# Performance work log

Measured on AMD Instinct MI355X. Metric: run time of the kernel, lower is better.

Reference implementation:

```python
import jax, jax.numpy as jnp
import numpy as np

B, C, L, D = 8, 32, 2048, 128
R, H = 8, 4  # num_routers, num_heads


def setup_inputs() -> dict:
    key = jax.random.key(0)
    ks = jax.random.split(key, 20)
    p = lambda k, shape: jax.random.normal(k, shape, dtype=jnp.float32) * 0.02
    inp = {
        "Z": jax.random.normal(ks[0], (B, C, L, D), dtype=jnp.float32),
        "router": p(ks[1], (R, D)),
        # router_sender projections (d_model -> d_model, torch Linear stored as x@W+b)
        "Wq1": p(ks[2], (D, D)), "bq1": jnp.zeros((D,), jnp.float32),
        "Wk1": p(ks[3], (D, D)), "bk1": jnp.zeros((D,), jnp.float32),
        "Wv1": p(ks[4], (D, D)), "bv1": jnp.zeros((D,), jnp.float32),
        "Wo1": p(ks[5], (D, D)), "bo1": jnp.zeros((D,), jnp.float32),
        # router_receiver projections
        "Wq2": p(ks[6], (D, D)), "bq2": jnp.zeros((D,), jnp.float32),
        "Wk2": p(ks[7], (D, D)), "bk2": jnp.zeros((D,), jnp.float32),
        "Wv2": p(ks[8], (D, D)), "bv2": jnp.zeros((D,), jnp.float32),
        "Wo2": p(ks[9], (D, D)), "bo2": jnp.zeros((D,), jnp.float32),
        # LayerNorm
        "gamma": jnp.ones((D,), jnp.float32),
        "beta": jnp.zeros((D,), jnp.float32),
    }
    return inp


def _cross_attn(q_in, k_in, v_in, Wq, bq, Wk, bk, Wv, bv, Wo, bo):
    # Informer FullAttention + AttentionLayer (dropout=0)
    Bn, Lq, Dm = q_in.shape
    Lk = k_in.shape[1]
    dh = Dm // H
    q = (q_in @ Wq + bq).reshape(Bn, Lq, H, dh)
    k = (k_in @ Wk + bk).reshape(Bn, Lk, H, dh)
    v = (v_in @ Wv + bv).reshape(Bn, Lk, H, dh)
    scale = 1.0 / np.sqrt(dh)
    scores = jnp.einsum("blhe,bshe->bhls", q, k) * scale
    A = jax.nn.softmax(scores, axis=-1)
    out = jnp.einsum("bhls,bshd->blhd", A, v).reshape(Bn, Lq, Dm)
    return out @ Wo + bo


def _layernorm(x, gamma, beta, eps=1e-5):
    mu = jnp.mean(x, axis=-1, keepdims=True)
    var = jnp.mean(jnp.square(x - mu), axis=-1, keepdims=True)
    return (x - mu) * jax.lax.rsqrt(var + eps) * gamma + beta


def reference(Z, router, Wq1, bq1, Wk1, bk1, Wv1, bv1, Wo1, bo1,
              Wq2, bq2, Wk2, bk2, Wv2, bv2, Wo2, bo2, gamma, beta):
    Bz, Cz, Lz, Dz = Z.shape
    x = Z.reshape(Bz * Cz, Lz, Dz)
    batch_router = jnp.broadcast_to(router[None], (Bz * Cz, R, Dz))
    # stage 1: routers attend to the sequence (R x L)
    router_buffer = _cross_attn(batch_router, x, x,
                                Wq1, bq1, Wk1, bk1, Wv1, bv1, Wo1, bo1)
    # stage 2: sequence attends to routers (L x R)
    router_receive = _cross_attn(x, router_buffer, router_buffer,
                                 Wq2, bq2, Wk2, bk2, Wv2, bv2, Wo2, bo2)
    out = _layernorm(x + router_receive, gamma, beta)
    return out.reshape(Bz, Cz, Lz, Dz)
```

## Files before the change

kernel.cpp:

```cpp
#include <hip/hip_runtime.h>

typedef float f4_t __attribute__((ext_vector_type(4)));
typedef __bf16 bf8_t __attribute__((ext_vector_type(8)));
typedef __bf16 bf4_t __attribute__((ext_vector_type(4)));

#define MFMA16(a,b,c) __builtin_amdgcn_mfma_f32_16x16x32_bf16((a),(b),(c),0,0,0)

static constexpr float kScale = 0.17677669529663687f;

__device__ __forceinline__ void bar_lds() {
  asm volatile("s_waitcnt lgkmcnt(0)" ::: "memory");
  __builtin_amdgcn_s_barrier();
}

__global__ __launch_bounds__(256) void k0_fold(
    const float* __restrict__ router, const float* __restrict__ Wq1,
    const float* __restrict__ bq1, const float* __restrict__ Wk1,
    const float* __restrict__ bk1, __bf16* __restrict__ q1t,
    float* __restrict__ c1)
{
  __shared__ float q1[8][132];
  const int t = threadIdx.x, b = blockIdx.x;
  {
    const int dp = t & 127, rh = t >> 7;
    float acc[4] = {0.f, 0.f, 0.f, 0.f};
#pragma unroll 4
    for (int e = 0; e < 128; ++e) {
      float wq = Wq1[e*128 + dp];
#pragma unroll
      for (int i = 0; i < 4; ++i)
        acc[i] += router[(rh*4 + i)*128 + e] * wq;
    }
#pragma unroll
    for (int i = 0; i < 4; ++i)
      q1[rh*4 + i][dp] = acc[i] + bq1[dp];
  }
  __syncthreads();
  {
    const int j = t & 31, h = j >> 3, r = j & 7;
    const int e = b*8 + (t >> 5);
    f4_t qv[8];
#pragma unroll
    for (int d4 = 0; d4 < 8; ++d4)
      qv[d4] = *(const f4_t*)&q1[r][h*32 + d4*4];
    float acc = 0.f;
#pragma unroll
    for (int d4 = 0; d4 < 8; ++d4) {
      f4_t wv = *(const f4_t*)(Wk1 + e*128 + h*32 + d4*4);
#pragma unroll
      for (int i = 0; i < 4; ++i) acc += qv[d4][i] * wv[i];
    }
    q1t[j*128 + e] = (__bf16)(acc * kScale);
  }
  if (b == 0 && t < 32) {
    int h = t >> 3, r = t & 7;
    float acc = 0.f;
    for (int d = 0; d < 32; ++d) acc += q1[r][h*32 + d] * bk1[h*32 + d];
    c1[t] = acc * kScale;
  }
}

__global__ __launch_bounds__(512) void k1_stage1(
    const float* __restrict__ Z, const __bf16* __restrict__ q1t_g,
    const float* __restrict__ c1_g, float* __restrict__ xap,
    float* __restrict__ lp, __bf16* __restrict__ xws)
{
  __shared__ __bf16 xb[64][136];
  __shared__ __bf16 xT[128][72];
  __shared__ __bf16 PT[32][72];
  __shared__ float lds_l[32];

  const int tid = threadIdx.x;
  const int bid = blockIdx.x;
  const float* xbase = Z + (size_t)bid * (256 * 128);
  __bf16* xwb = xws + (size_t)bid * (256 * 128);

  if (tid < 32) lds_l[tid] = 0.f;

  const int lane = tid & 63;
  const int w = tid >> 6;
  const int lc = lane & 15;
  const int lg = lane >> 4;
  const int ms = w >> 2;
  const int ns = w & 3;
  float c1v[4];
#pragma unroll
  for (int r2 = 0; r2 < 4; ++r2) c1v[r2] = c1_g[ms*16 + lg*4 + r2];
  bf8_t aq[4];
#pragma unroll
  for (int ks = 0; ks < 4; ++ks)
    aq[ks] = *(const bf8_t*)(q1t_g + (ms*16 + lc)*128 + ks*32 + lg*8);

  const f4_t fzero = {0.f, 0.f, 0.f, 0.f};
  f4_t accxa[2] = { fzero, fzero };
  float Lacc[4] = {0.f, 0.f, 0.f, 0.f};

  const int srow = tid >> 4;
  const int sd0  = (tid & 15) << 3;

  f4_t zr[4];
#pragma unroll
  for (int i = 0; i < 2; ++i) {
    const float* p = xbase + (srow + 32*i)*128 + sd0;
    zr[i*2]   = __builtin_nontemporal_load((const f4_t*)p);
    zr[i*2+1] = __builtin_nontemporal_load((const f4_t*)(p + 4));
  }

  bar_lds();

  for (int tile = 0; tile < 4; ++tile) {
#pragma unroll
    for (int i = 0; i < 2; ++i) {
      int pos = srow + 32*i;
      f4_t v0 = zr[i*2], v1 = zr[i*2+1];
      bf8_t b8 = { (__bf16)v0.x, (__bf16)v0.y, (__bf16)v0.z, (__bf16)v0.w,
                   (__bf16)v1.x, (__bf16)v1.y, (__bf16)v1.z, (__bf16)v1.w };
      *(bf8_t*)&xb[pos][sd0] = b8;
      *(bf8_t*)(xwb + (tile*64 + pos)*128 + sd0) = b8;
    }
    bar_lds();

    if (tile < 3) {
      const float* xt = xbase + (tile + 1) * (64 * 128);
#pragma unroll
      for (int i = 0; i < 2; ++i) {
        const float* p = xt + (srow + 32*i)*128 + sd0;
        zr[i*2]   = __builtin_nontemporal_load((const f4_t*)p);
        zr[i*2+1] = __builtin_nontemporal_load((const f4_t*)(p + 4));
      }
    }

#pragma unroll
    for (int s = 0; s < 2; ++s) {
      int u = tid + s*512;
      int dim = u & 127, pb = (u >> 7) << 3;
      bf8_t t8;
#pragma unroll
      for (int p = 0; p < 8; ++p) t8[p] = xb[pb + p][dim];
      *(bf8_t*)&xT[dim][pb] = t8;
    }
    f4_t sacc = fzero;
#pragma unroll
    for (int ks = 0; ks < 4; ++ks) {
      bf8_t b = *(const bf8_t*)&xb[ns*16 + lc][ks*32 + lg*8];
      sacc = MFMA16(aq[ks], b, sacc);
    }
    const int posn = ns*16 + lc;
#pragma unroll
    for (int r2 = 0; r2 < 4; ++r2) {
      float p = __expf(sacc[r2] + c1v[r2]);
      Lacc[r2] += p;
      PT[ms*16 + lg*4 + r2][posn] = (__bf16)p;
    }
    bar_lds();

#pragma unroll
    for (int nt = 0; nt < 2; ++nt) {
      const int dimt = (ns << 1) + nt;
#pragma unroll
      for (int ks = 0; ks < 2; ++ks) {
        bf8_t a = *(const bf8_t*)&xT[dimt*16 + lc][ks*32 + lg*8];
        bf8_t b = *(const bf8_t*)&PT[ms*16 + lc][ks*32 + lg*8];
        accxa[nt] = MFMA16(a, b, accxa[nt]);
      }
    }
  }

#pragma unroll
  for (int r2 = 0; r2 < 4; ++r2) {
    float v = Lacc[r2];
    v += __shfl_xor(v, 1);
    v += __shfl_xor(v, 2);
    v += __shfl_xor(v, 4);
    v += __shfl_xor(v, 8);
    if (lc == 0) atomicAdd(&lds_l[ms*16 + lg*4 + r2], v);
  }
  bar_lds();

  float* xo = xap + (size_t)bid * 4096;
  const int jrow = ms*16 + lc;
#pragma unroll
  for (int nt = 0; nt < 2; ++nt) {
    const int dim0 = ((ns << 1) + nt)*16 + lg*4;
    *(f4_t*)(xo + jrow*128 + dim0) = accxa[nt];
  }
  if (tid < 32) lp[bid*32 + tid] = lds_l[tid];
}

__global__ __launch_bounds__(512) void k2_stage2(
    const __bf16* __restrict__ xws, const float* __restrict__ xap,
    const float* __restrict__ lp,
    const float* __restrict__ Wv1, const float* __restrict__ bv1,
    const float* __restrict__ Wo1, const float* __restrict__ bo1,
    const float* __restrict__ Wk2, const float* __restrict__ bk2,
    const float* __restrict__ Wv2, const float* __restrict__ bv2,
    const float* __restrict__ Wq2, const float* __restrict__ bq2,
    const float* __restrict__ Wo2, const float* __restrict__ bo2,
    const float* __restrict__ gamma, const float* __restrict__ beta,
    float* __restrict__ out)
{
  __shared__ __align__(16) char smem[64896];
  __bf16 (*xb)[136]  = (__bf16 (*)[136])(smem);
  __bf16 (*P2)[40]   = (__bf16 (*)[40])(smem + 34816);
  __bf16 (*ktL)[136] = (__bf16 (*)[136])(smem + 45056);
  __bf16 (*vtL)[40]  = (__bf16 (*)[40])(smem + 53760);
  float* c2L  = (float*)(smem + 64000);
  float* invl = (float*)(smem + 64128);
  float (*xaT)[33]   = (float (*)[33])(smem);
  float (*out1T)[13] = (float (*)[13])(smem + 16896);
  float (*rbT)[13]   = (float (*)[13])(smem + 23552);
  float (*k2s)[140]  = (float (*)[140])(smem);
  float (*v2s)[140]  = (float (*)[140])(smem + 4480);

  const int tid = threadIdx.x;
  const int blk = blockIdx.x;
  const int batch = blk >> 1;

  const int lane = tid & 63;
  const int w = tid >> 6;
  const int lc = lane & 15;
  const int lg = lane >> 4;

  int spos[4], sd[4];
#pragma unroll
  for (int j = 0; j < 4; ++j) {
    int c = lane + j*64;
    spos[j] = w*16 + (c >> 4);
    sd[j]   = (c & 15) << 3;
  }
  const size_t base0 = (size_t)blk * 8 * 16384;
  uint4 zx[4];
#pragma unroll
  for (int j = 0; j < 4; ++j)
    zx[j] = *(const uint4*)(xws + base0 + spos[j]*128 + sd[j]);

#pragma unroll
  for (int i = 0; i < 8; ++i) {
    int idx = tid + i*512;
    int j = idx >> 7, e = idx & 127;
    float s = 0.f;
#pragma unroll
    for (int k = 0; k < 8; ++k)
      s += xap[(size_t)(batch*8 + k) * 4096 + idx];
    xaT[e][j] = s;
  }
  if (tid < 32) {
    float s = 0.f;
#pragma unroll
    for (int k = 0; k < 8; ++k) s += lp[(batch*8 + k)*32 + tid];
    invl[tid] = 1.f / s;
  }
  bar_lds();
  {
    const int hd = tid & 127, rh = tid >> 7, h = hd >> 5;
    const int j0 = h*8 + rh*2;
    float acc[2] = {0.f, 0.f};
#pragma unroll 4
    for (int e = 0; e < 128; ++e) {
      float wv = Wv1[e*128 + hd];
      acc[0] += xaT[e][j0] * wv;
      acc[1] += xaT[e][j0 + 1] * wv;
    }
    float bv = bv1[hd];
    out1T[hd][rh*2]     = acc[0] * invl[j0] + bv;
    out1T[hd][rh*2 + 1] = acc[1] * invl[j0 + 1] + bv;
  }
  bar_lds();
  {
    const int e2 = tid & 127, rh = tid >> 7;
    float acc[2] = {0.f, 0.f};
#pragma unroll 4
    for (int hd = 0; hd < 128; ++hd) {
      float wo = Wo1[hd*128 + e2];
      acc[0] += out1T[hd][rh*2] * wo;
      acc[1] += out1T[hd][rh*2 + 1] * wo;
    }
    float bo = bo1[e2];
    rbT[e2][rh*2]     = acc[0] + bo;
    rbT[e2][rh*2 + 1] = acc[1] + bo;
  }
  bar_lds();
  {
    const int hd = tid & 127, q = tid >> 7;
    const int sel = q >> 1, r0 = (q & 1) * 4;
    const float* W  = sel ? Wv2 : Wk2;
    const float* bb = sel ? bv2 : bk2;
    float (*dst)[140] = sel ? v2s : k2s;
    float bbv = bb[hd];
    float acc[4] = {bbv, bbv, bbv, bbv};
#pragma unroll 4
    for (int e = 0; e < 128; ++e) {
      float wv = W[e*128 + hd];
#pragma unroll
      for (int i = 0; i < 4; ++i) acc[i] += rbT[e][r0 + i] * wv;
    }
#pragma unroll
    for (int i = 0; i < 4; ++i) dst[r0 + i][hd] = acc[i];
  }
  bar_lds();
  {
    const int j = tid & 31, h = j >> 3, r = j & 7;
    const int esub = tid >> 5;
    f4_t k2v[8], v2v[8];
#pragma unroll
    for (int d4 = 0; d4 < 8; ++d4) {
      k2v[d4] = *(const f4_t*)&k2s[r][h*32 + d4*4];
      v2v[d4] = *(const f4_t*)&v2s[r][h*32 + d4*4];
    }
#pragma unroll
    for (int ei = 0; ei < 8; ++ei) {
      const int e = esub + ei*16;
      float acck = 0.f, accv = 0.f;
#pragma unroll
      for (int d4 = 0; d4 < 8; ++d4) {
        f4_t wq = *(const f4_t*)(Wq2 + e*128 + h*32 + d4*4);
#pragma unroll
        for (int i = 0; i < 4; ++i) {
          acck += wq[i] * k2v[d4][i];
          accv += v2v[d4][i] * Wo2[(h*32 + d4*4 + i)*128 + e];
        }
      }
      ktL[j][e] = (__bf16)(acck * kScale);
      vtL[e][j] = (__bf16)accv;
    }
    if (tid < 32) {
      int hh = tid >> 3, rr = tid & 7;
      float acc = 0.f;
#pragma unroll
      for (int d = 0; d < 32; ++d) acc += bq2[hh*32 + d] * k2s[rr][hh*32 + d];
      c2L[tid] = acc * kScale;
    }
  }
  bar_lds();

  float c2v[2] = { c2L[lc], c2L[16 + lc] };
  f4_t bo2v[8], gv[8], bv[8];
#pragma unroll
  for (int nt = 0; nt < 8; ++nt) {
    int dd = nt*16 + lg*4;
    bo2v[nt] = *(const f4_t*)(bo2 + dd);
    gv[nt]   = *(const f4_t*)(gamma + dd);
    bv[nt]   = *(const f4_t*)(beta + dd);
  }
  bf8_t vfrag[8];
#pragma unroll
  for (int nt = 0; nt < 8; ++nt)
    vfrag[nt] = *(const bf8_t*)&vtL[nt*16 + lc][lg*8];

  const f4_t fzero = {0.f, 0.f, 0.f, 0.f};

  for (int c = 0; c < 8; ++c) {
    const size_t cb = base0 + (size_t)c * 16384;
#pragma unroll
    for (int j = 0; j < 4; ++j)
      *(uint4*)&xb[spos[j]][sd[j]] = zx[j];
    if (c < 7) {
#pragma unroll
      for (int j = 0; j < 4; ++j)
        zx[j] = *(const uint4*)(xws + cb + 16384 + spos[j]*128 + sd[j]);
    }

    f4_t sacc[2] = { fzero, fzero };
#pragma unroll
    for (int ks = 0; ks < 4; ++ks) {
      bf8_t a = *(const bf8_t*)&xb[w*16 + lc][ks*32 + lg*8];
#pragma unroll
      for (int nt = 0; nt < 2; ++nt) {
        bf8_t b = *(const bf8_t*)&ktL[nt*16 + lc][ks*32 + lg*8];
        sacc[nt] = MFMA16(a, b, sacc[nt]);
      }
    }
#pragma unroll
    for (int nt = 0; nt < 2; ++nt) {
#pragma unroll
      for (int r2 = 0; r2 < 4; ++r2) {
        float p = __expf(sacc[nt][r2] + c2v[nt]);
        float sum = p;
        sum += __shfl_xor(sum, 1);
        sum += __shfl_xor(sum, 2);
        sum += __shfl_xor(sum, 4);
        P2[w*16 + lg*4 + r2][nt*16 + lc] = (__bf16)(p * __builtin_amdgcn_rcpf(sum));
      }
    }

    bf8_t pf = *(const bf8_t*)&P2[w*16 + lc][lg*8];
    f4_t racc[8];
#pragma unroll
    for (int nt = 0; nt < 8; ++nt)
      racc[nt] = MFMA16(vfrag[nt], pf, fzero);

    const int pos = w*16 + lc;
    float s1 = 0.f, s2 = 0.f;
#pragma unroll
    for (int nt = 0; nt < 8; ++nt) {
      bf4_t xq = *(const bf4_t*)&xb[pos][nt*16 + lg*4];
#pragma unroll
      for (int r = 0; r < 4; ++r) {
        float tv = racc[nt][r] + bo2v[nt][r] + (float)xq[r];
        racc[nt][r] = tv;
        s1 += tv; s2 += tv*tv;
      }
    }
    s1 += __shfl_xor(s1, 16); s1 += __shfl_xor(s1, 32);
    s2 += __shfl_xor(s2, 16); s2 += __shfl_xor(s2, 32);
    float mean = s1 * (1.f/128.f);
    float var = s2 * (1.f/128.f) - mean*mean;
    float rstd = rsqrtf(var + 1e-5f);

    float* y = out + cb + (size_t)pos*128;
#pragma unroll
    for (int nt = 0; nt < 8; ++nt) {
      f4_t o;
#pragma unroll
      for (int r = 0; r < 4; ++r)
        o[r] = (racc[nt][r] - mean) * rstd * gv[nt][r] + bv[nt][r];
      *(f4_t*)(y + nt*16 + lg*4) = o;
    }
  }
}

extern "C" void kernel_launch(void* const* d_in, const int* in_sizes, int n_in,
                              void* d_out, int out_size, void* d_ws, size_t ws_size,
                              hipStream_t stream)
{
  const float* Z     = (const float*)d_in[0];
  const float* router= (const float*)d_in[1];
  const float* Wq1   = (const float*)d_in[2];
  const float* bq1   = (const float*)d_in[3];
  const float* Wk1   = (const float*)d_in[4];
  const float* bk1   = (const float*)d_in[5];
  const float* Wv1   = (const float*)d_in[6];
  const float* bv1   = (const float*)d_in[7];
  const float* Wo1   = (const float*)d_in[8];
  const float* bo1   = (const float*)d_in[9];
  const float* Wq2   = (const float*)d_in[10];
  const float* bq2   = (const float*)d_in[11];
  const float* Wk2   = (const float*)d_in[12];
  const float* bk2   = (const float*)d_in[13];
  const float* Wv2   = (const float*)d_in[14];
  const float* bv2   = (const float*)d_in[15];
  const float* Wo2   = (const float*)d_in[16];
  const float* bo2   = (const float*)d_in[17];
  const float* gamma = (const float*)d_in[18];
  const float* beta  = (const float*)d_in[19];
  float* out = (float*)d_out;

  char* base = (char*)d_ws;
  __bf16* q1tb = (__bf16*)(base);
  float*  c1   = (float*)(base + 8192);
  float*  lp   = (float*)(base + 65536);
  float*  xap  = (float*)(base + (1u<<20));
  __bf16* xws  = (__bf16*)(base + (40u<<20));
  (void)in_sizes; (void)n_in; (void)out_size; (void)ws_size;

  k0_fold<<<dim3(16), dim3(256), 0, stream>>>(router, Wq1, bq1, Wk1, bk1, q1tb, c1);
  k1_stage1<<<dim3(2048), dim3(512), 0, stream>>>(Z, q1tb, c1, xap, lp, xws);
  k2_stage2<<<dim3(512), dim3(512), 0, stream>>>(xws, xap, lp,
                                                 Wv1, bv1, Wo1, bo1,
                                                 Wk2, bk2, Wv2, bv2,
                                                 Wq2, bq2, Wo2,
                                                 bo2, gamma, beta, out);
}
```

Measured before the change: 314.3 us.

## Move stage-2 key/value fragments from LDS to global workspace, stream output stores

The stage-2 kernel now writes the folded key and value matrices for the receiver attention to a global workspace instead of LDS, then reads them straight from global memory inside the chunk loop. This cuts the kernel's LDS footprint. The bo2/gamma/beta vectors and the value fragments are reloaded per iteration instead of held in registers, which lowers register pressure. Output stores become nontemporal. The trade-off is extra global/L1 traffic in the inner loop, plus both blocks of a batch writing identical workspace data, in exchange for possibly higher occupancy and less cache pollution from the output.

Result: faster. 265.6 us (median of 2 runs) (-15.5%).

```diff
diff --git a/kernel.cpp b/kernel.cpp
--- a/kernel.cpp
+++ b/kernel.cpp
@@ -10,6 +10,10 @@
 
 __device__ __forceinline__ void bar_lds() {
   asm volatile("s_waitcnt lgkmcnt(0)" ::: "memory");
+  __builtin_amdgcn_s_barrier();
+}
+__device__ __forceinline__ void bar_full() {
+  asm volatile("s_waitcnt vmcnt(0) lgkmcnt(0)" ::: "memory");
   __builtin_amdgcn_s_barrier();
 }
 
@@ -197,15 +201,13 @@
     const float* __restrict__ Wq2, const float* __restrict__ bq2,
     const float* __restrict__ Wo2, const float* __restrict__ bo2,
     const float* __restrict__ gamma, const float* __restrict__ beta,
-    float* __restrict__ out)
+    __bf16* kt2g, __bf16* vt2g, float* __restrict__ out)
 {
-  __shared__ __align__(16) char smem[64896];
+  __shared__ __align__(16) char smem[45312];
   __bf16 (*xb)[136]  = (__bf16 (*)[136])(smem);
   __bf16 (*P2)[40]   = (__bf16 (*)[40])(smem + 34816);
-  __bf16 (*ktL)[136] = (__bf16 (*)[136])(smem + 45056);
-  __bf16 (*vtL)[40]  = (__bf16 (*)[40])(smem + 53760);
-  float* c2L  = (float*)(smem + 64000);
-  float* invl = (float*)(smem + 64128);
+  float* c2L  = (float*)(smem + 45056);
+  float* invl = (float*)(smem + 45184);
   float (*xaT)[33]   = (float (*)[33])(smem);
   float (*out1T)[13] = (float (*)[13])(smem + 16896);
   float (*rbT)[13]   = (float (*)[13])(smem + 23552);
@@ -320,8 +322,8 @@
           accv += v2v[d4][i] * Wo2[(h*32 + d4*4 + i)*128 + e];
         }
       }
-      ktL[j][e] = (__bf16)(acck * kScale);
-      vtL[e][j] = (__bf16)accv;
+      kt2g[(size_t)batch*4096 + j*128 + e] = (__bf16)(acck * kScale);
+      vt2g[(size_t)batch*4096 + e*32 + j] = (__bf16)accv;
     }
     if (tid < 32) {
       int hh = tid >> 3, rr = tid & 7;
@@ -331,21 +333,11 @@
       c2L[tid] = acc * kScale;
     }
   }
-  bar_lds();
-
+  bar_full();
+
+  const __bf16* ktb = kt2g + (size_t)batch * 4096;
+  const __bf16* vtb = vt2g + (size_t)batch * 4096;
   float c2v[2] = { c2L[lc], c2L[16 + lc] };
-  f4_t bo2v[8], gv[8], bv[8];
-#pragma unroll
-  for (int nt = 0; nt < 8; ++nt) {
-    int dd = nt*16 + lg*4;
-    bo2v[nt] = *(const f4_t*)(bo2 + dd);
-    gv[nt]   = *(const f4_t*)(gamma + dd);
-    bv[nt]   = *(const f4_t*)(beta + dd);
-  }
-  bf8_t vfrag[8];
-#pragma unroll
-  for (int nt = 0; nt < 8; ++nt)
-    vfrag[nt] = *(const bf8_t*)&vtL[nt*16 + lc][lg*8];
 
   const f4_t fzero = {0.f, 0.f, 0.f, 0.f};
 
@@ -366,7 +358,7 @@
       bf8_t a = *(const bf8_t*)&xb[w*16 + lc][ks*32 + lg*8];
 #pragma unroll
       for (int nt = 0; nt < 2; ++nt) {
-        bf8_t b = *(const bf8_t*)&ktL[nt*16 + lc][ks*32 + lg*8];
+        bf8_t b = *(const bf8_t*)(ktb + (nt*16 + lc)*128 + ks*32 + lg*8);
         sacc[nt] = MFMA16(a, b, sacc[nt]);
       }
     }
@@ -386,17 +378,20 @@
     bf8_t pf = *(const bf8_t*)&P2[w*16 + lc][lg*8];
     f4_t racc[8];
 #pragma unroll
-    for (int nt = 0; nt < 8; ++nt)
-      racc[nt] = MFMA16(vfrag[nt], pf, fzero);
+    for (int nt = 0; nt < 8; ++nt) {
+      bf8_t vfr = *(const bf8_t*)(vtb + (nt*16 + lc)*32 + lg*8);
+      racc[nt] = MFMA16(vfr, pf, fzero);
+    }
 
     const int pos = w*16 + lc;
     float s1 = 0.f, s2 = 0.f;
 #pragma unroll
     for (int nt = 0; nt < 8; ++nt) {
       bf4_t xq = *(const bf4_t*)&xb[pos][nt*16 + lg*4];
+      f4_t bq = *(const f4_t*)(bo2 + nt*16 + lg*4);
 #pragma unroll
       for (int r = 0; r < 4; ++r) {
-        float tv = racc[nt][r] + bo2v[nt][r] + (float)xq[r];
+        float tv = racc[nt][r] + bq[r] + (float)xq[r];
         racc[nt][r] = tv;
         s1 += tv; s2 += tv*tv;
       }
@@ -410,11 +405,13 @@
     float* y = out + cb + (size_t)pos*128;
 #pragma unroll
     for (int nt = 0; nt < 8; ++nt) {
+      f4_t gq = *(const f4_t*)(gamma + nt*16 + lg*4);
+      f4_t bb = *(const f4_t*)(beta + nt*16 + lg*4);
       f4_t o;
 #pragma unroll
       for (int r = 0; r < 4; ++r)
-        o[r] = (racc[nt][r] - mean) * rstd * gv[nt][r] + bv[nt][r];
-      *(f4_t*)(y + nt*16 + lg*4) = o;
+        o[r] = (racc[nt][r] - mean) * rstd * gq[r] + bb[r];
+      __builtin_nontemporal_store(o, (f4_t*)(y + nt*16 + lg*4));
     }
   }
 }
@@ -450,6 +447,8 @@
   float*  c1   = (float*)(base + 8192);
   float*  lp   = (float*)(base + 65536);
   float*  xap  = (float*)(base + (1u<<20));
+  __bf16* kt2b = (__bf16*)(base + (36u<<20));
+  __bf16* vt2b = (__bf16*)(base + (38u<<20));
   __bf16* xws  = (__bf16*)(base + (40u<<20));
   (void)in_sizes; (void)n_in; (void)out_size; (void)ws_size;
 
@@ -459,5 +458,6 @@
                                                  Wv1, bv1, Wo1, bo1,
                                                  Wk2, bk2, Wv2, bv2,
                                                  Wq2, bq2, Wo2,
-                                                 bo2, gamma, beta, out);
-}
+                                                 bo2, gamma, beta,
+                                                 kt2b, vt2b, out);
+}
```
